# Performance work log

Hardware: AMD Instinct MI355X
Metric: run time of the kernel (lower is better)

Reference implementation:

```python
import jax, jax.numpy as jnp
import numpy as np

EPS = 1e-5
B, NG, D, DR, NF, NA, LG = 4096, 1440, 50, 222, 8000, 64, 3

def _conv1d(x, w, b, s):
    # x: [N,C,L], w: [O,I,K]
    y = jax.lax.conv_general_dilated(x, w, (s,), 'VALID', dimension_numbers=('NCH', 'OIH', 'NCH'))
    return y + b[None, :, None]

def _bn(x, g, b):
    # training-mode BatchNorm1d over (N, L) per channel
    m = jnp.mean(x, axis=(0, 2), keepdims=True)
    v = jnp.var(x, axis=(0, 2), keepdims=True)
    return (x - m) * jax.lax.rsqrt(v + EPS) * g[None, :, None] + b[None, :, None]

def _maxpool(x, k, s):
    return jax.lax.reduce_window(x, -jnp.inf, jax.lax.max, (1, 1, k), (1, 1, s), 'VALID')

def setup_inputs() -> dict:
    key = jax.random.key(0)
    ks = jax.random.split(key, 24)
    inp = {}
    inp['rma'] = jax.random.normal(ks[0], (B, NG), jnp.float32)
    inp['var'] = jax.random.uniform(ks[1], (B, NG), jnp.float32)
    inp['drug_id'] = jax.random.randint(ks[2], (B,), 0, DR)
    inp['fuse_weight'] = 0.5 + 0.25 * jax.random.normal(ks[3], (DR, NG), jnp.float32)
    inp['sim_softmax'] = jax.nn.softmax(jax.random.normal(ks[4], (DR, DR), jnp.float32), axis=1)
    inp['embed_table'] = 0.1 * jax.random.normal(ks[5], (NF, D), jnp.float32)
    inp['gnn_W'] = 0.1 * jax.random.normal(ks[6], (LG, D, D), jnp.float32)
    inp['gnn_b'] = jnp.zeros((LG, D), jnp.float32)
    inp['fingerprints'] = jax.random.randint(ks[7], (DR, NA), 0, NF)
    A = (jax.random.uniform(ks[8], (DR, NA, NA)) < 0.1).astype(jnp.float32)
    inp['adjacency'] = jnp.maximum(A, A.transpose(0, 2, 1))
    inp['conv1_w'] = 0.1 * jax.random.normal(ks[9], (10, 1, 15), jnp.float32)
    inp['conv1_b'] = jnp.zeros((10,), jnp.float32)
    inp['bn1_g'] = jnp.ones((10,), jnp.float32); inp['bn1_b'] = jnp.zeros((10,), jnp.float32)
    inp['conv2_w'] = 0.1 * jax.random.normal(ks[10], (5, 10, 15), jnp.float32)
    inp['conv2_b'] = jnp.zeros((5,), jnp.float32)
    inp['bn2_g'] = jnp.ones((5,), jnp.float32); inp['bn2_b'] = jnp.zeros((5,), jnp.float32)
    inp['lin_gene_w'] = 0.1 * jax.random.normal(ks[11], (70, 32), jnp.float32)
    inp['lin_gene_b'] = jnp.zeros((32,), jnp.float32)
    inp['mlin_w'] = 0.1 * jax.random.normal(ks[12], (210, 100), jnp.float32)
    inp['mlin_b'] = jnp.zeros((100,), jnp.float32)
    inp['mconv1_w'] = 0.1 * jax.random.normal(ks[13], (5, 1, 10), jnp.float32)
    inp['mconv1_b'] = jnp.zeros((5,), jnp.float32)
    inp['mbn1_g'] = jnp.ones((5,), jnp.float32); inp['mbn1_b'] = jnp.zeros((5,), jnp.float32)
    inp['mconv2_w'] = 0.1 * jax.random.normal(ks[14], (5, 5, 10), jnp.float32)
    inp['mconv2_b'] = jnp.zeros((5,), jnp.float32)
    inp['mbn2_g'] = jnp.ones((5,), jnp.float32); inp['mbn2_b'] = jnp.zeros((5,), jnp.float32)
    inp['out_w'] = 0.1 * jax.random.normal(ks[15], (5, 1), jnp.float32)
    inp['out_b'] = jnp.zeros((1,), jnp.float32)
    return inp

def reference(rma, var, drug_id, fuse_weight, sim_softmax, embed_table, gnn_W, gnn_b,
              fingerprints, adjacency, conv1_w, conv1_b, bn1_g, bn1_b,
              conv2_w, conv2_b, bn2_g, bn2_b, lin_gene_w, lin_gene_b,
              mlin_w, mlin_b, mconv1_w, mconv1_b, mbn1_g, mbn1_b,
              mconv2_w, mconv2_b, mbn2_g, mbn2_b, out_w, out_b):
    # combine: clamp fuse_weight, attention = (sim[drug] @ fuse_weight) * var, z = rma + attention
    fw = jnp.clip(fuse_weight, 0.0, 1.0)                       # [DR,NG]
    com = rma + (sim_softmax[drug_id] @ fw) * var              # [B,NG]
    # gene CNN branch (dropout = identity / eval)
    x = com[:, None, :]                                        # [B,1,NG]
    x = jax.nn.relu(_bn(_conv1d(x, conv1_w, conv1_b, 2), bn1_g, bn1_b))   # [B,10,713]
    x = jax.nn.relu(_bn(_conv1d(x, conv2_w, conv2_b, 2), bn2_g, bn2_b))   # [B,5,350]
    x = _maxpool(x, 5, 5)                                      # [B,5,70]
    x = jax.nn.relu(jnp.einsum('bcl,lo->bco', x, lin_gene_w) + lin_gene_b)  # [B,5,32]
    out_gene = x.reshape(x.shape[0], -1)                       # [B,160]
    # GNN compound branch: batched dense-adjacency message passing
    xs = embed_table[fingerprints[drug_id]]                    # [B,NA,D]
    A = adjacency[drug_id]                                     # [B,NA,NA]
    for i in range(gnn_W.shape[0]):
        hs = jax.nn.relu(jnp.einsum('bnd,de->bne', xs, gnn_W[i]) + gnn_b[i])
        xs = xs + jnp.einsum('bnm,bmd->bnd', A, hs)
    compound = jnp.mean(xs, axis=1)                            # [B,D]
    # merged head
    concat = jnp.concatenate([out_gene, compound], axis=1)     # [B,210]
    m = jnp.tanh(concat @ mlin_w + mlin_b)[:, None, :]         # [B,1,100]
    m = _maxpool(_bn(_conv1d(m, mconv1_w, mconv1_b, 2), mbn1_g, mbn1_b), 3, 3)  # [B,5,15]
    m = _maxpool(_bn(_conv1d(m, mconv2_w, mconv2_b, 2), mbn2_g, mbn2_b), 3, 3)  # [B,5,1]
    y = m.reshape(m.shape[0], -1) @ out_w + out_b              # [B,1]
    return y
```

## Files before the change

### kernel.cpp

```cpp
#include <hip/hip_runtime.h>

#define EPS 1e-5f

#define B_   4096
#define NG_  1440
#define DR_  222
#define D_   50
#define NA_  64
#define LG_  3
#define L1_  713
#define C1_  10
#define K1_  15
#define L2_  350
#define C2_  5
#define LP_  70
#define LO_  32
#define CAT_ 210
#define M_   100
#define LM1_ 46
#define PM1_ 15
#define LM2_ 3

#define NEO_ 722
#define X1ST_ 360

__global__ __launch_bounds__(256) void k_fuse(
    const float* __restrict__ fw, const float* __restrict__ sim,
    float* __restrict__ P)
{
  const int d0 = blockIdx.x * 2;
  const int g = blockIdx.y * 256 + threadIdx.x;
  const int tid = threadIdx.x;
  __shared__ float s0[DR_], s1[DR_];
  for (int r = tid; r < DR_; r += 256) {
    s0[r] = sim[d0 * DR_ + r];
    s1[r] = sim[(d0 + 1) * DR_ + r];
  }
  __syncthreads();
  if (g >= NG_) return;
  float a0 = 0.f, a1 = 0.f;
#pragma unroll 6
  for (int r = 0; r < DR_; ++r) {
    float w = fw[r * NG_ + g];
    w = fminf(fmaxf(w, 0.f), 1.f);
    a0 += s0[r] * w;
    a1 += s1[r] * w;
  }
  P[d0 * NG_ + g] = a0;
  P[(d0 + 1) * NG_ + g] = a1;
}

__global__ __launch_bounds__(256) void k_gnn(
    const float* __restrict__ embed, const float* __restrict__ gW,
    const float* __restrict__ gb, const int* __restrict__ fp,
    const float* __restrict__ adj, float* __restrict__ compound)
{
  const int d = blockIdx.x;
  const int tid = threadIdx.x;
  const int wid = tid >> 6, lane = tid & 63;
  __shared__ __align__(16) float WT[D_ * 52];
  __shared__ __align__(16) float hsl[NA_ * 52];
  __shared__ float xsl[NA_ * 53];
  __shared__ float bl[D_];
  __shared__ int fps[NA_];

  if (tid < NA_) fps[tid] = fp[d * NA_ + tid];
  if (wid == 0) { hsl[lane * 52 + 50] = 0.f; hsl[lane * 52 + 51] = 0.f; }
  __syncthreads();

  float xs[52];
  const float* erow = embed + (size_t)fps[lane] * D_;
#pragma unroll
  for (int j = 0; j < D_; ++j) xs[j] = erow[j];
  xs[50] = 0.f; xs[51] = 0.f;
  float Ar[NA_];
  const float* arow = adj + (size_t)d * NA_ * NA_ + lane * NA_;
#pragma unroll
  for (int j = 0; j < NA_; ++j) Ar[j] = arow[j];

  const int e0 = (wid < 2) ? wid * 13 : 26 + (wid - 2) * 12;
  const int ecnt = (wid < 2) ? 13 : 12;

  for (int layer = 0; layer < LG_; ++layer) {
    const float* Wg = gW + layer * D_ * D_;
    for (int i = tid; i < D_ * 52; i += 256) {
      int e = i / 52, dd = i - e * 52;
      WT[i] = (dd < D_) ? Wg[dd * D_ + e] : 0.f;
    }
    if (tid < D_) bl[tid] = gb[layer * D_ + tid];
    __syncthreads();

    for (int ei = 0; ei < ecnt; ++ei) {
      int e = e0 + ei;
      float c0 = bl[e], c1 = 0.f, c2 = 0.f, c3 = 0.f;
#pragma unroll
      for (int c = 0; c < 13; ++c) {
        float4 wv = *(const float4*)&WT[e * 52 + 4 * c];
        c0 += xs[4 * c + 0] * wv.x;
        c1 += xs[4 * c + 1] * wv.y;
        c2 += xs[4 * c + 2] * wv.z;
        c3 += xs[4 * c + 3] * wv.w;
      }
      hsl[lane * 52 + e] = fmaxf((c0 + c1) + (c2 + c3), 0.f);
    }
    __syncthreads();

    for (int c = wid; c < 13; c += 4) {
      float a0 = 0.f, a1 = 0.f, a2 = 0.f, a3 = 0.f;
#pragma unroll
      for (int m = 0; m < NA_; ++m) {
        float4 hv = *(const float4*)&hsl[m * 52 + 4 * c];
        float am = Ar[m];
        a0 += am * hv.x; a1 += am * hv.y; a2 += am * hv.z; a3 += am * hv.w;
      }
      int dd = 4 * c;
      xsl[lane * 53 + dd + 0] = xs[dd + 0] + a0;
      xsl[lane * 53 + dd + 1] = xs[dd + 1] + a1;
      if (dd + 2 < D_) {
        xsl[lane * 53 + dd + 2] = xs[dd + 2] + a2;
        xsl[lane * 53 + dd + 3] = xs[dd + 3] + a3;
      }
    }
    __syncthreads();
#pragma unroll
    for (int j = 0; j < D_; ++j) xs[j] = xsl[lane * 53 + j];
    __syncthreads();
  }

  if (wid == 0 && lane < D_) {
    float s = 0.f;
    for (int n = 0; n < NA_; ++n) s += xsl[n * 53 + lane];
    compound[d * D_ + lane] = s * (1.f / NA_);
  }
}

__global__ __launch_bounds__(384, 6) void k_conv1(
    const float* __restrict__ rma, const float* __restrict__ varr,
    const int* __restrict__ did, const float* __restrict__ P,
    const float* __restrict__ w1g, const float* __restrict__ b1g,
    float* __restrict__ comg, float* __restrict__ part1)
{
  const int b = blockIdx.x, tid = threadIdx.x;
  const int wid = tid >> 6;
  __shared__ float comE[NEO_], comO[NEO_];
  __shared__ float red[6][C1_ * 2];
  const int dd = did[b];

  for (int g = tid; g < NG_; g += 384) {
    float v = rma[b * NG_ + g] + P[dd * NG_ + g] * varr[b * NG_ + g];
    comg[b * NG_ + g] = v;
    if (g & 1) comO[g >> 1] = v; else comE[g >> 1] = v;
  }
  if (tid < 2) { comE[720 + tid] = 0.f; comO[720 + tid] = 0.f; }
  __syncthreads();

  float s1[C1_], s2[C1_];
#pragma unroll
  for (int c = 0; c < C1_; ++c) { s1[c] = 0.f; s2[c] = 0.f; }
  if (tid < 357) {
    float wE[9], wO[8];
#pragma unroll
    for (int m = 0; m < 9; ++m) wE[m] = comE[2 * tid + m];
#pragma unroll
    for (int m = 0; m < 8; ++m) wO[m] = comO[2 * tid + m];
    const bool two = (tid < 356);
#pragma unroll
    for (int c = 0; c < C1_; ++c) {
      float a0 = b1g[c], a1 = a0;
#pragma unroll
      for (int m = 0; m < 8; ++m) {
        float w = w1g[c * K1_ + 2 * m];
        a0 += w * wE[m]; a1 += w * wE[m + 1];
      }
#pragma unroll
      for (int m = 0; m < 7; ++m) {
        float w = w1g[c * K1_ + 2 * m + 1];
        a0 += w * wO[m]; a1 += w * wO[m + 1];
      }
      s1[c] = a0; s2[c] = a0 * a0;
      if (two) { s1[c] += a1; s2[c] += a1 * a1; }
    }
  }
#pragma unroll
  for (int c = 0; c < C1_; ++c) {
#pragma unroll
    for (int off = 32; off > 0; off >>= 1) {
      s1[c] += __shfl_down(s1[c], off, 64);
      s2[c] += __shfl_down(s2[c], off, 64);
    }
  }
  if ((tid & 63) == 0) {
#pragma unroll
    for (int c = 0; c < C1_; ++c) {
      red[wid][c * 2 + 0] = s1[c];
      red[wid][c * 2 + 1] = s2[c];
    }
  }
  __syncthreads();
  if (tid < C1_ * 2) {
    float S = 0.f;
#pragma unroll
    for (int w = 0; w < 6; ++w) S += red[w][tid];
    part1[b * (C1_ * 2) + tid] = S;
  }
}

__global__ __launch_bounds__(256) void k_bnfin(
    const float* __restrict__ part, int nblk, int C, float N,
    const float* __restrict__ g, const float* __restrict__ bta,
    float* __restrict__ ac)
{
  const int c = blockIdx.x, tid = threadIdx.x;
  float s1 = 0.f, s2 = 0.f;
  for (int j = tid; j < nblk; j += 256) {
    s1 += part[(j * C + c) * 2 + 0];
    s2 += part[(j * C + c) * 2 + 1];
  }
#pragma unroll
  for (int off = 32; off > 0; off >>= 1) {
    s1 += __shfl_down(s1, off, 64);
    s2 += __shfl_down(s2, off, 64);
  }
  __shared__ float r1[4], r2[4];
  int w = tid >> 6;
  if ((tid & 63) == 0) { r1[w] = s1; r2[w] = s2; }
  __syncthreads();
  if (tid == 0) {
    float S1 = r1[0] + r1[1] + r1[2] + r1[3];
    float S2 = r2[0] + r2[1] + r2[2] + r2[3];
    float mean = S1 / N;
    float v = S2 / N - mean * mean;
    float a = g[c] * rsqrtf(v + EPS);
    ac[c] = a;
    ac[C + c] = bta[c] - mean * a;
  }
}

__global__ __launch_bounds__(192, 4) void k_conv2(
    const float* __restrict__ comg, const float* __restrict__ w1g,
    const float* __restrict__ b1g, const float* __restrict__ ac1,
    const float* __restrict__ w2g, const float* __restrict__ b2g,
    float* __restrict__ x2g, float* __restrict__ part2)
{
  const int b = blockIdx.x, tid = threadIdx.x;
  const int wid = tid >> 6;
  __shared__ float x1E[C1_ * X1ST_], x1O[C1_ * X1ST_];
  __shared__ float red[3][C2_ * 2];

#pragma unroll 1
  for (int j = tid; j < 357; j += 192) {
    const float* base = comg + (size_t)b * NG_ + 4 * j;
    float4 v0 = *(const float4*)(base + 0);
    float4 v1 = *(const float4*)(base + 4);
    float4 v2 = *(const float4*)(base + 8);
    float4 v3 = *(const float4*)(base + 12);
    const bool two = (j < 356);
    float wE[9], wO[8];
    wE[0] = v0.x; wE[1] = v0.z; wE[2] = v1.x; wE[3] = v1.z;
    wE[4] = v2.x; wE[5] = v2.z; wE[6] = v3.x; wE[7] = v3.z;
    wE[8] = two ? base[16] : 0.f;
    wO[0] = v0.y; wO[1] = v0.w; wO[2] = v1.y; wO[3] = v1.w;
    wO[4] = v2.y; wO[5] = v2.w; wO[6] = v3.y; wO[7] = v3.w;
#pragma unroll 1
    for (int c = 0; c < C1_; ++c) {
      float a0 = b1g[c], a1 = a0;
#pragma unroll
      for (int m = 0; m < 8; ++m) {
        float w = w1g[c * K1_ + 2 * m];
        a0 += w * wE[m]; a1 += w * wE[m + 1];
      }
#pragma unroll
      for (int m = 0; m < 7; ++m) {
        float w = w1g[c * K1_ + 2 * m + 1];
        a0 += w * wO[m]; a1 += w * wO[m + 1];
      }
      float sc = ac1[c], sh = ac1[C1_ + c];
      x1E[c * X1ST_ + j] = fmaxf(sc * a0 + sh, 0.f);
      if (two) x1O[c * X1ST_ + j] = fmaxf(sc * a1 + sh, 0.f);
    }
  }
  __syncthreads();

  float A0[C2_], A1[C2_];
#pragma unroll
  for (int co = 0; co < C2_; ++co) { A0[co] = 0.f; A1[co] = 0.f; }
  if (tid < 175) {
#pragma unroll 1
    for (int ci = 0; ci < C1_; ++ci) {
      float xE[9], xO[8];
#pragma unroll
      for (int m = 0; m < 9; ++m) xE[m] = x1E[ci * X1ST_ + 2 * tid + m];
#pragma unroll
      for (int m = 0; m < 8; ++m) xO[m] = x1O[ci * X1ST_ + 2 * tid + m];
#pragma unroll
      for (int co = 0; co < C2_; ++co) {
#pragma unroll
        for (int m = 0; m < 8; ++m) {
          float w = w2g[(co * C1_ + ci) * K1_ + 2 * m];
          A0[co] += w * xE[m]; A1[co] += w * xE[m + 1];
        }
#pragma unroll
        for (int m = 0; m < 7; ++m) {
          float w = w2g[(co * C1_ + ci) * K1_ + 2 * m + 1];
          A0[co] += w * xO[m]; A1[co] += w * xO[m + 1];
        }
      }
    }
  }

  float t1[C2_], t2[C2_];
#pragma unroll
  for (int co = 0; co < C2_; ++co) { t1[co] = 0.f; t2[co] = 0.f; }
  if (tid < 175) {
#pragma unroll
    for (int co = 0; co < C2_; ++co) {
      float o0 = A0[co] + b2g[co];
      float o1 = A1[co] + b2g[co];
      *(float2*)&x2g[b * (C2_ * L2_) + co * L2_ + 2 * tid] = make_float2(o0, o1);
      t1[co] = o0 + o1; t2[co] = o0 * o0 + o1 * o1;
    }
  }
#pragma unroll
  for (int co = 0; co < C2_; ++co) {
#pragma unroll
    for (int off = 32; off > 0; off >>= 1) {
      t1[co] += __shfl_down(t1[co], off, 64);
      t2[co] += __shfl_down(t2[co], off, 64);
    }
  }
  if ((tid & 63) == 0) {
#pragma unroll
    for (int co = 0; co < C2_; ++co) {
      red[wid][co * 2 + 0] = t1[co];
      red[wid][co * 2 + 1] = t2[co];
    }
  }
  __syncthreads();
  if (tid < C2_ * 2) {
    float S = red[0][tid] + red[1][tid] + red[2][tid];
    part2[b * (C2_ * 2) + tid] = S;
  }
}

__global__ __launch_bounds__(256) void k_gene(
    const float* __restrict__ x2g, const float* __restrict__ ac2,
    const int* __restrict__ did, const float* __restrict__ compound,
    const float* __restrict__ lgwg, const float* __restrict__ lgbg,
    const float* __restrict__ mwg, const float* __restrict__ mbg,
    const float* __restrict__ mw1g, const float* __restrict__ mb1g,
    float* __restrict__ mraw1, float* __restrict__ partm1)
{
  const int b = blockIdx.x, tid = threadIdx.x;
  __shared__ float pooled[C2_ * LP_];
  __shared__ float lgw[LP_ * LO_];
  __shared__ float cat[CAT_];
  __shared__ float mv[M_];
  __shared__ float red1[C2_ * LM1_], red2[C2_ * LM1_];
  __shared__ float a2s[C2_], c2s[C2_];
  if (tid < C2_) { a2s[tid] = ac2[tid]; c2s[tid] = ac2[C2_ + tid]; }
  for (int i = tid; i < LP_ * LO_; i += 256) lgw[i] = lgwg[i];
  __syncthreads();
  for (int i = tid; i < C2_ * LP_; i += 256) {
    int c = i / LP_, p = i - c * LP_;
    const float* xr = x2g + (size_t)b * (C2_ * L2_) + c * L2_ + 5 * p;
    float aa = a2s[c], cc = c2s[c];
    float m = aa * xr[0] + cc;
    m = fmaxf(m, aa * xr[1] + cc);
    m = fmaxf(m, aa * xr[2] + cc);
    m = fmaxf(m, aa * xr[3] + cc);
    m = fmaxf(m, aa * xr[4] + cc);
    pooled[i] = fmaxf(m, 0.f);
  }
  __syncthreads();
  if (tid < 160) {
    int c = tid >> 5, o = tid & 31;
    float a = lgbg[o];
    for (int l = 0; l < LP_; ++l) a += pooled[c * LP_ + l] * lgw[l * LO_ + o];
    cat[tid] = fmaxf(a, 0.f);
  } else if (tid < CAT_) {
    cat[tid] = compound[did[b] * D_ + (tid - 160)];
  }
  __syncthreads();
  if (tid < M_) {
    float a = mbg[tid];
    for (int i = 0; i < CAT_; ++i) a += cat[i] * mwg[i * M_ + tid];
    mv[tid] = tanhf(a);
  }
  __syncthreads();
  if (tid < C2_ * LM1_) {
    int c = tid / LM1_, t = tid - c * LM1_;
    float a = mb1g[c];
#pragma unroll
    for (int k = 0; k < 10; ++k) a += mw1g[c * 10 + k] * mv[2 * t + k];
    mraw1[b * (C2_ * LM1_) + c * LM1_ + t] = a;
    red1[tid] = a;
    red2[tid] = a * a;
  }
  __syncthreads();
  if (tid < C2_) {
    float S1 = 0.f, S2 = 0.f;
    for (int j = 0; j < LM1_; ++j) { S1 += red1[tid * LM1_ + j]; S2 += red2[tid * LM1_ + j]; }
    partm1[(b * C2_ + tid) * 2 + 0] = S1;
    partm1[(b * C2_ + tid) * 2 + 1] = S2;
  }
}

__global__ __launch_bounds__(256) void k_mhead2(
    const float* __restrict__ mraw1, const float* __restrict__ acm1,
    const float* __restrict__ mw2g, const float* __restrict__ mb2g,
    float* __restrict__ mraw2, float* __restrict__ partm2)
{
  const int tid = threadIdx.x;
  const int b = blockIdx.x * 256 + tid;
  __shared__ float w2[C2_ * C2_ * 10];
  __shared__ float a1[C2_], c1[C2_], b2s[C2_];
  __shared__ float rw1[C2_][4], rw2[C2_][4];
  if (tid < C2_ * C2_ * 10) w2[tid] = mw2g[tid];
  if (tid < C2_) { a1[tid] = acm1[tid]; c1[tid] = acm1[C2_ + tid]; b2s[tid] = mb2g[tid]; }
  __syncthreads();
  float p[C2_ * PM1_];
  const float* row = mraw1 + (size_t)b * (C2_ * LM1_);
#pragma unroll
  for (int c = 0; c < C2_; ++c) {
    float ac = a1[c], cc = c1[c];
#pragma unroll
    for (int q = 0; q < PM1_; ++q) {
      float m = ac * row[c * LM1_ + 3 * q] + cc;
      m = fmaxf(m, ac * row[c * LM1_ + 3 * q + 1] + cc);
      m = fmaxf(m, ac * row[c * LM1_ + 3 * q + 2] + cc);
      p[c * PM1_ + q] = m;
    }
  }
#pragma unroll
  for (int co = 0; co < C2_; ++co) {
    float t1 = 0.f, t2 = 0.f;
#pragma unroll
    for (int l = 0; l < LM2_; ++l) {
      float a = b2s[co];
#pragma unroll
      for (int ci = 0; ci < C2_; ++ci)
#pragma unroll
        for (int k = 0; k < 10; ++k)
          a += w2[(co * C2_ + ci) * 10 + k] * p[ci * PM1_ + 2 * l + k];
      mraw2[b * (C2_ * LM2_) + co * LM2_ + l] = a;
      t1 += a; t2 += a * a;
    }
#pragma unroll
    for (int off = 32; off > 0; off >>= 1) {
      t1 += __shfl_down(t1, off, 64);
      t2 += __shfl_down(t2, off, 64);
    }
    if ((tid & 63) == 0) { rw1[co][tid >> 6] = t1; rw2[co][tid >> 6] = t2; }
  }
  __syncthreads();
  if (tid < C2_ * 2) {
    int co = tid >> 1, s = tid & 1;
    float S = 0.f;
#pragma unroll
    for (int w = 0; w < 4; ++w) S += (s ? rw2[co][w] : rw1[co][w]);
    partm2[blockIdx.x * (C2_ * 2) + tid] = S;
  }
}

__global__ __launch_bounds__(256) void k_final(
    const float* __restrict__ mraw2, const float* __restrict__ acm2,
    const float* __restrict__ owg, const float* __restrict__ obg,
    float* __restrict__ out)
{
  const int b = blockIdx.x * 256 + threadIdx.x;
  float y = obg[0];
#pragma unroll
  for (int c = 0; c < C2_; ++c) {
    float a = acm2[c], cc = acm2[C2_ + c];
    float m = a * mraw2[b * 15 + c * 3 + 0] + cc;
    m = fmaxf(m, a * mraw2[b * 15 + c * 3 + 1] + cc);
    m = fmaxf(m, a * mraw2[b * 15 + c * 3 + 2] + cc);
    y += owg[c] * m;
  }
  out[b] = y;
}

extern "C" void kernel_launch(void* const* d_in, const int* in_sizes, int n_in,
                              void* d_out, int out_size, void* d_ws, size_t ws_size,
                              hipStream_t stream) {
  (void)in_sizes; (void)n_in; (void)out_size; (void)ws_size;
  const float* rma   = (const float*)d_in[0];
  const float* varr  = (const float*)d_in[1];
  const int*   did   = (const int*)d_in[2];
  const float* fw    = (const float*)d_in[3];
  const float* sim   = (const float*)d_in[4];
  const float* embed = (const float*)d_in[5];
  const float* gW    = (const float*)d_in[6];
  const float* gb    = (const float*)d_in[7];
  const int*   fp    = (const int*)d_in[8];
  const float* adj   = (const float*)d_in[9];
  const float* w1g   = (const float*)d_in[10];
  const float* b1g   = (const float*)d_in[11];
  const float* bn1g  = (const float*)d_in[12];
  const float* bn1b  = (const float*)d_in[13];
  const float* w2g   = (const float*)d_in[14];
  const float* b2g   = (const float*)d_in[15];
  const float* bn2g  = (const float*)d_in[16];
  const float* bn2b  = (const float*)d_in[17];
  const float* lgwg  = (const float*)d_in[18];
  const float* lgbg  = (const float*)d_in[19];
  const float* mwg   = (const float*)d_in[20];
  const float* mbg   = (const float*)d_in[21];
  const float* mw1g  = (const float*)d_in[22];
  const float* mb1g  = (const float*)d_in[23];
  const float* mbn1g = (const float*)d_in[24];
  const float* mbn1b = (const float*)d_in[25];
  const float* mw2g  = (const float*)d_in[26];
  const float* mb2g  = (const float*)d_in[27];
  const float* mbn2g = (const float*)d_in[28];
  const float* mbn2b = (const float*)d_in[29];
  const float* owg   = (const float*)d_in[30];
  const float* obg   = (const float*)d_in[31];
  float* out = (float*)d_out;

  float* ws = (float*)d_ws;
  size_t o = 0;
  float* P        = ws + o; o += (size_t)DR_ * NG_;
  float* compound = ws + o; o += (size_t)DR_ * D_;
  float* comg     = ws + o; o += (size_t)B_ * NG_;
  float* part1    = ws + o; o += (size_t)B_ * C1_ * 2;
  float* ac1      = ws + o; o += 2 * C1_;
  float* x2g      = ws + o; o += (size_t)B_ * C2_ * L2_;
  float* part2    = ws + o; o += (size_t)B_ * C2_ * 2;
  float* ac2      = ws + o; o += 2 * C2_;
  float* mraw1    = ws + o; o += (size_t)B_ * C2_ * LM1_;
  float* partm1   = ws + o; o += (size_t)B_ * C2_ * 2;
  float* acm1     = ws + o; o += 2 * C2_;
  float* mraw2    = ws + o; o += (size_t)B_ * C2_ * LM2_;
  float* partm2   = ws + o; o += 16 * C2_ * 2;
  float* acm2     = ws + o; o += 2 * C2_;

  hipLaunchKernelGGL(k_fuse, dim3(DR_ / 2, 6), dim3(256), 0, stream, fw, sim, P);
  hipLaunchKernelGGL(k_gnn, dim3(DR_), dim3(256), 0, stream,
                     embed, gW, gb, fp, adj, compound);
  hipLaunchKernelGGL(k_conv1, dim3(B_), dim3(384), 0, stream,
                     rma, varr, did, P, w1g, b1g, comg, part1);
  hipLaunchKernelGGL(k_bnfin, dim3(C1_), dim3(256), 0, stream,
                     part1, B_, C1_, (float)B_ * (float)L1_, bn1g, bn1b, ac1);
  hipLaunchKernelGGL(k_conv2, dim3(B_), dim3(192), 0, stream,
                     comg, w1g, b1g, ac1, w2g, b2g, x2g, part2);
  hipLaunchKernelGGL(k_bnfin, dim3(C2_), dim3(256), 0, stream,
                     part2, B_, C2_, (float)B_ * (float)L2_, bn2g, bn2b, ac2);
  hipLaunchKernelGGL(k_gene, dim3(B_), dim3(256), 0, stream,
                     x2g, ac2, did, compound, lgwg, lgbg, mwg, mbg, mw1g, mb1g,
                     mraw1, partm1);
  hipLaunchKernelGGL(k_bnfin, dim3(C2_), dim3(256), 0, stream,
                     partm1, B_, C2_, (float)B_ * (float)LM1_, mbn1g, mbn1b, acm1);
  hipLaunchKernelGGL(k_mhead2, dim3(16), dim3(256), 0, stream,
                     mraw1, acm1, mw2g, mb2g, mraw2, partm2);
  hipLaunchKernelGGL(k_bnfin, dim3(C2_), dim3(256), 0, stream,
                     partm2, 16, C2_, (float)B_ * (float)LM2_, mbn2g, mbn2b, acm2);
  hipLaunchKernelGGL(k_final, dim3(16), dim3(256), 0, stream,
                     mraw2, acm2, owg, obg, out);
}
```

Baseline: 245.2 us.

## Load conv1 inputs directly into registers with float4 and split mlin reduction

k_conv1 no longer stages the fused gene vector in shared memory. Each thread now loads its 17-element window directly from global memory with float4 loads, computes the fused values in registers, and writes its slice of comg. This removes the shared-memory staging and one barrier, at the cost of overlapping redundant global reads across neighbouring threads and more register pressure, with the occupancy hint lowered from 6 to 4. In k_gene the 210-long mlin dot product is split across 200 threads in two halves and combined through shared memory before the tanh.

```diff
diff --git a/kernel.cpp b/kernel.cpp
--- a/kernel.cpp
+++ b/kernel.cpp
@@ -21,7 +21,6 @@
 #define PM1_ 15
 #define LM2_ 3
 
-#define NEO_ 722
 #define X1ST_ 360
 
 __global__ __launch_bounds__(256) void k_fuse(
@@ -134,7 +133,7 @@
   }
 }
 
-__global__ __launch_bounds__(384, 6) void k_conv1(
+__global__ __launch_bounds__(384, 4) void k_conv1(
     const float* __restrict__ rma, const float* __restrict__ varr,
     const int* __restrict__ did, const float* __restrict__ P,
     const float* __restrict__ w1g, const float* __restrict__ b1g,
@@ -142,28 +141,36 @@
 {
   const int b = blockIdx.x, tid = threadIdx.x;
   const int wid = tid >> 6;
-  __shared__ float comE[NEO_], comO[NEO_];
   __shared__ float red[6][C1_ * 2];
   const int dd = did[b];
-
-  for (int g = tid; g < NG_; g += 384) {
-    float v = rma[b * NG_ + g] + P[dd * NG_ + g] * varr[b * NG_ + g];
-    comg[b * NG_ + g] = v;
-    if (g & 1) comO[g >> 1] = v; else comE[g >> 1] = v;
-  }
-  if (tid < 2) { comE[720 + tid] = 0.f; comO[720 + tid] = 0.f; }
-  __syncthreads();
+  const float* rb = rma  + (size_t)b * NG_ + 4 * tid;
+  const float* vb = varr + (size_t)b * NG_ + 4 * tid;
+  const float* pp = P    + (size_t)dd * NG_ + 4 * tid;
 
   float s1[C1_], s2[C1_];
 #pragma unroll
   for (int c = 0; c < C1_; ++c) { s1[c] = 0.f; s2[c] = 0.f; }
+
   if (tid < 357) {
+    float4 r0 = *(const float4*)(rb + 0),  r1 = *(const float4*)(rb + 4);
+    float4 r2 = *(const float4*)(rb + 8),  r3 = *(const float4*)(rb + 12);
+    float4 v0 = *(const float4*)(vb + 0),  v1 = *(const float4*)(vb + 4);
+    float4 v2 = *(const float4*)(vb + 8),  v3 = *(const float4*)(vb + 12);
+    float4 p0 = *(const float4*)(pp + 0),  p1 = *(const float4*)(pp + 4);
+    float4 p2 = *(const float4*)(pp + 8),  p3 = *(const float4*)(pp + 12);
+    const bool two = (tid < 356);
     float wE[9], wO[8];
-#pragma unroll
-    for (int m = 0; m < 9; ++m) wE[m] = comE[2 * tid + m];
-#pragma unroll
-    for (int m = 0; m < 8; ++m) wO[m] = comO[2 * tid + m];
-    const bool two = (tid < 356);
+    wE[0] = r0.x + p0.x * v0.x;  wO[0] = r0.y + p0.y * v0.y;
+    wE[1] = r0.z + p0.z * v0.z;  wO[1] = r0.w + p0.w * v0.w;
+    wE[2] = r1.x + p1.x * v1.x;  wO[2] = r1.y + p1.y * v1.y;
+    wE[3] = r1.z + p1.z * v1.z;  wO[3] = r1.w + p1.w * v1.w;
+    wE[4] = r2.x + p2.x * v2.x;  wO[4] = r2.y + p2.y * v2.y;
+    wE[5] = r2.z + p2.z * v2.z;  wO[5] = r2.w + p2.w * v2.w;
+    wE[6] = r3.x + p3.x * v3.x;  wO[6] = r3.y + p3.y * v3.y;
+    wE[7] = r3.z + p3.z * v3.z;  wO[7] = r3.w + p3.w * v3.w;
+    wE[8] = two ? (rb[16] + pp[16] * vb[16]) : 0.f;
+    *(float4*)&comg[(size_t)b * NG_ + 4 * tid] =
+        make_float4(wE[0], wO[0], wE[1], wO[1]);
 #pragma unroll
     for (int c = 0; c < C1_; ++c) {
       float a0 = b1g[c], a1 = a0;
@@ -180,7 +187,15 @@
       s1[c] = a0; s2[c] = a0 * a0;
       if (two) { s1[c] += a1; s2[c] += a1 * a1; }
     }
-  }
+  } else if (tid < 360) {
+    float4 r0 = *(const float4*)(rb);
+    float4 v0 = *(const float4*)(vb);
+    float4 p0 = *(const float4*)(pp);
+    *(float4*)&comg[(size_t)b * NG_ + 4 * tid] =
+        make_float4(r0.x + p0.x * v0.x, r0.y + p0.y * v0.y,
+                    r0.z + p0.z * v0.z, r0.w + p0.w * v0.w);
+  }
+
 #pragma unroll
   for (int c = 0; c < C1_; ++c) {
 #pragma unroll
@@ -355,6 +370,7 @@
   __shared__ float lgw[LP_ * LO_];
   __shared__ float cat[CAT_];
   __shared__ float mv[M_];
+  __shared__ float mvp[2][M_];
   __shared__ float red1[C2_ * LM1_], red2[C2_ * LM1_];
   __shared__ float a2s[C2_], c2s[C2_];
   if (tid < C2_) { a2s[tid] = ac2[tid]; c2s[tid] = ac2[C2_ + tid]; }
@@ -381,11 +397,15 @@
     cat[tid] = compound[did[b] * D_ + (tid - 160)];
   }
   __syncthreads();
-  if (tid < M_) {
-    float a = mbg[tid];
-    for (int i = 0; i < CAT_; ++i) a += cat[i] * mwg[i * M_ + tid];
-    mv[tid] = tanhf(a);
-  }
+  if (tid < 200) {
+    int half = tid / 100, o = tid - half * 100;
+    float a = 0.f;
+    int i0 = half * 105;
+    for (int i = i0; i < i0 + 105; ++i) a += cat[i] * mwg[i * M_ + o];
+    mvp[half][o] = a;
+  }
+  __syncthreads();
+  if (tid < M_) mv[tid] = tanhf(mvp[0][tid] + mvp[1][tid] + mbg[tid]);
   __syncthreads();
   if (tid < C2_ * LM1_) {
     int c = tid / LM1_, t = tid - c * LM1_;
```

Result: faster. 238.3 us (-2.8%).
